# Optimization experiments

Hardware: AMD Instinct MI355X
Metric: run time of the kernel (lower is better)

## Reference

```python
import jax, jax.numpy as jnp
import numpy as np

D_MODEL = 1024
N_HEADS = 16
CAUSAL = True
NEG_INF = -1e10


def get_freqs(seq_len, n_dim):
    # standard RoPE frequencies: theta_i = 10000^(-2i/n_dim), angles[s, i] = s * theta_i
    inv_freq = 1.0 / (10000.0 ** (jnp.arange(0, n_dim, 2, dtype=jnp.float32) / n_dim))
    t = jnp.arange(seq_len, dtype=jnp.float32)
    return jnp.outer(t, inv_freq)  # [S, n_dim//2]


def rope(x, freqs):
    # x: [B, S, H, n_dim]; interleaved pair rotation
    B, S, H, Dh = x.shape
    xr = x.reshape(B, S, H, Dh // 2, 2)
    x1, x2 = xr[..., 0], xr[..., 1]
    cos = jnp.cos(freqs)[None, :, None, :]  # [1,S,1,Dh/2]
    sin = jnp.sin(freqs)[None, :, None, :]
    o1 = x1 * cos - x2 * sin
    o2 = x1 * sin + x2 * cos
    return jnp.stack([o1, o2], axis=-1).reshape(B, S, H, Dh)


def setup_inputs() -> dict:
    key = jax.random.key(0)
    ks = jax.random.split(key, 5)
    B, S, D = 2, 2048, D_MODEL
    return {
        "x": jax.random.normal(ks[0], (B, S, D), dtype=jnp.float32),
        "qw": jax.random.normal(ks[1], (D, D), dtype=jnp.float32),
        "kw": jax.random.normal(ks[2], (D, D), dtype=jnp.float32),
        "vw": jax.random.normal(ks[3], (D, D), dtype=jnp.float32),
        "ow": jax.random.normal(ks[4], (D, D), dtype=jnp.float32),
    }


def reference(x, qw, kw, vw, ow):
    B, S, D = x.shape
    H = N_HEADS
    Dh = D // H
    Q = (x @ qw).reshape(B, S, H, Dh)
    K = (x @ kw).reshape(B, S, H, Dh)
    V = (x @ vw).reshape(B, S, H, Dh)
    freqs = get_freqs(S, Dh)
    Q = rope(Q, freqs)
    K = rope(K, freqs)
    # [B,H,S,S] scores, scaled by sqrt(d_model) as in the original (not sqrt(head_dim))
    scores = jnp.einsum("bqhd,bkhd->bhqk", Q, K) / jnp.sqrt(jnp.float32(D))
    scores = scores.astype(jnp.float32)
    if CAUSAL:
        causal = jnp.tril(jnp.ones((S, S), dtype=bool))
        scores = jnp.where(causal[None, None, :, :], scores, NEG_INF)
    weights = jax.nn.softmax(scores, axis=-1)
    attn = jnp.einsum("bhqk,bkhd->bqhd", weights, V).reshape(B, S, D)
    return attn @ ow
```

## Files before the change

kernel.cpp:

```cpp
#include <hip/hip_runtime.h>
#include <hip/hip_bf16.h>
#include <math.h>

#define SEQ    2048
#define BATCH  2
#define DM     1024
#define NH     16
#define DH     64
#define BS_ROWS 4096
#define KDIM   1024

typedef __attribute__((ext_vector_type(8))) short short8v;
typedef __attribute__((ext_vector_type(4))) float f32x4;
typedef unsigned short ushort_t;

__device__ __forceinline__ unsigned short f2bf(float f) {
  union { float f; unsigned u; } v; v.f = f;
  unsigned r = (v.u + 0x7FFF + ((v.u >> 16) & 1)) >> 16;
  return (unsigned short)r;
}
__device__ __forceinline__ float bf2f(unsigned short h) {
  union { unsigned u; float f; } v; v.u = ((unsigned)h) << 16;
  return v.f;
}

__device__ __forceinline__ void gl16(const void* g, void* l) {
  __builtin_amdgcn_global_load_lds(
      (const __attribute__((address_space(1))) unsigned int*)g,
      (__attribute__((address_space(3))) unsigned int*)l,
      16, 0, 0);
}

__global__ __launch_bounds__(256)
void split_f32(const float* __restrict__ src, ushort_t* __restrict__ h,
               ushort_t* __restrict__ l, int n8)
{
  const int i = blockIdx.x * 256 + threadIdx.x;
  if (i >= n8) return;
  const float4 v0 = ((const float4*)src)[2 * i];
  const float4 v1 = ((const float4*)src)[2 * i + 1];
  const float vals[8] = {v0.x, v0.y, v0.z, v0.w, v1.x, v1.y, v1.z, v1.w};
  short8v hv, lv;
  #pragma unroll
  for (int e = 0; e < 8; e++) {
    const unsigned short hb = f2bf(vals[e]);
    hv[e] = (short)hb;
    lv[e] = (short)f2bf(vals[e] - bf2f(hb));
  }
  ((short8v*)h)[i] = hv;
  ((short8v*)l)[i] = lv;
}

__global__ __launch_bounds__(256)
void wtrans(const float* __restrict__ w0, const float* __restrict__ w1,
            const float* __restrict__ w2, const float* __restrict__ w3,
            ushort_t* __restrict__ WT)
{
  __shared__ float tile[64][65];
  const int z = blockIdx.z;
  const float* __restrict__ W = (z == 0) ? w0 : (z == 1) ? w1 : (z == 2) ? w2 : w3;
  ushort_t* __restrict__ Oh = WT + (size_t)z * 2097152;
  ushort_t* __restrict__ Ol = Oh + 1048576;

  const int n0 = blockIdx.x * 64, k0 = blockIdx.y * 64;
  const int r  = threadIdx.x >> 2;
  const int c0 = (threadIdx.x & 3) * 16;

  #pragma unroll
  for (int i = 0; i < 4; i++) {
    const float4 v = *(const float4*)&W[(size_t)(k0 + r) * KDIM + n0 + c0 + 4 * i];
    tile[r][c0 + 4 * i + 0] = v.x; tile[r][c0 + 4 * i + 1] = v.y;
    tile[r][c0 + 4 * i + 2] = v.z; tile[r][c0 + 4 * i + 3] = v.w;
  }
  __syncthreads();

  #pragma unroll
  for (int c = 0; c < 2; c++) {
    short8v hv, lv;
    #pragma unroll
    for (int e = 0; e < 8; e++) {
      const float x = tile[c0 + c * 8 + e][r];
      const unsigned short hb = f2bf(x);
      hv[e] = (short)hb;
      lv[e] = (short)f2bf(x - bf2f(hb));
    }
    const size_t off = (size_t)(n0 + r) * KDIM + k0 + c0 + c * 8;
    *(short8v*)&Oh[off] = hv;
    if (z <= 2) *(short8v*)&Ol[off] = lv;
  }
}

#define MF(a_, b_, c_) __builtin_amdgcn_mfma_f32_16x16x32_bf16(a_, b_, c_, 0, 0, 0)

#define M16(p_, q_)                                                          \
  c00=MF(p_##0,q_##0,c00); c01=MF(p_##0,q_##1,c01); c02=MF(p_##0,q_##2,c02); c03=MF(p_##0,q_##3,c03); \
  c10=MF(p_##1,q_##0,c10); c11=MF(p_##1,q_##1,c11); c12=MF(p_##1,q_##2,c12); c13=MF(p_##1,q_##3,c13); \
  c20=MF(p_##2,q_##0,c20); c21=MF(p_##2,q_##1,c21); c22=MF(p_##2,q_##2,c22); c23=MF(p_##2,q_##3,c23); \
  c30=MF(p_##3,q_##0,c30); c31=MF(p_##3,q_##1,c31); c32=MF(p_##3,q_##2,c32); c33=MF(p_##3,q_##3,c33);

__global__ __launch_bounds__(256, 2)
void gemm_qkv(const ushort_t* __restrict__ Ahp, const ushort_t* __restrict__ Alp,
              const ushort_t* __restrict__ WT,
              ushort_t* __restrict__ Qh, ushort_t* __restrict__ Ql,
              ushort_t* __restrict__ Kh, ushort_t* __restrict__ Kl,
              ushort_t* __restrict__ Vt)
{
  const int mode = blockIdx.z;
  const bool qk = (mode <= 1);
  const ushort_t* __restrict__ Bhp = WT + (size_t)mode * 2097152;
  const ushort_t* __restrict__ Blp = Bhp + 1048576;

  __shared__ ushort_t A2[128][64];
  __shared__ ushort_t B2[128][64];

  const int t = threadIdx.x;
  const int lane = t & 63, w = t >> 6;
  const int l4 = lane & 15, lh = lane >> 4;
  const int wm = w >> 1, wn = w & 1;

  const int lin = blockIdx.x + (blockIdx.y << 3);
  const int sw  = ((lin & 7) << 5) + (lin >> 3);
  const int row0 = (sw >> 3) * 128, col0 = (sw & 7) * 128;

  const int srow = t >> 3;
  const int spc  = t & 7;
  const int slc  = spc ^ (srow & 7);
  const int koff = (slc & 3) * 8;
  const ushort_t* __restrict__ sA = (slc < 4) ? Ahp : Alp;
  const ushort_t* __restrict__ sB = (slc < 4) ? Bhp : (qk ? Blp : Bhp);

  const int pcA = lh ^ (l4 & 7);

  f32x4 c00 = {0,0,0,0}, c01 = {0,0,0,0}, c02 = {0,0,0,0}, c03 = {0,0,0,0};
  f32x4 c10 = {0,0,0,0}, c11 = {0,0,0,0}, c12 = {0,0,0,0}, c13 = {0,0,0,0};
  f32x4 c20 = {0,0,0,0}, c21 = {0,0,0,0}, c22 = {0,0,0,0}, c23 = {0,0,0,0};
  f32x4 c30 = {0,0,0,0}, c31 = {0,0,0,0}, c32 = {0,0,0,0}, c33 = {0,0,0,0};

  const int rA = wm * 64 + l4;
  const int rB = wn * 64 + l4;

  for (int k0 = 0; k0 < KDIM; k0 += 32) {
    #pragma unroll
    for (int i = 0; i < 4; i++) {
      gl16(sA + (size_t)(row0 + i * 32 + srow) * KDIM + k0 + koff,
           (char*)A2 + i * 4096 + w * 1024);
      gl16(sB + (size_t)(col0 + i * 32 + srow) * KDIM + k0 + koff,
           (char*)B2 + i * 4096 + w * 1024);
    }
    __syncthreads();

    const short8v ah0 = *(const short8v*)&A2[rA +  0][pcA * 8];
    const short8v ah1 = *(const short8v*)&A2[rA + 16][pcA * 8];
    const short8v ah2 = *(const short8v*)&A2[rA + 32][pcA * 8];
    const short8v ah3 = *(const short8v*)&A2[rA + 48][pcA * 8];
    const short8v al0 = *(const short8v*)&A2[rA +  0][(pcA ^ 4) * 8];
    const short8v al1 = *(const short8v*)&A2[rA + 16][(pcA ^ 4) * 8];
    const short8v al2 = *(const short8v*)&A2[rA + 32][(pcA ^ 4) * 8];
    const short8v al3 = *(const short8v*)&A2[rA + 48][(pcA ^ 4) * 8];
    const short8v bh0 = *(const short8v*)&B2[rB +  0][pcA * 8];
    const short8v bh1 = *(const short8v*)&B2[rB + 16][pcA * 8];
    const short8v bh2 = *(const short8v*)&B2[rB + 32][pcA * 8];
    const short8v bh3 = *(const short8v*)&B2[rB + 48][pcA * 8];

    M16(ah, bh)
    if (qk) {
      const short8v bl0 = *(const short8v*)&B2[rB +  0][(pcA ^ 4) * 8];
      const short8v bl1 = *(const short8v*)&B2[rB + 16][(pcA ^ 4) * 8];
      const short8v bl2 = *(const short8v*)&B2[rB + 32][(pcA ^ 4) * 8];
      const short8v bl3 = *(const short8v*)&B2[rB + 48][(pcA ^ 4) * 8];
      M16(ah, bl)
    }
    M16(al, bh)
    __syncthreads();
  }

  f32x4 acc[4][4];
  acc[0][0]=c00; acc[0][1]=c01; acc[0][2]=c02; acc[0][3]=c03;
  acc[1][0]=c10; acc[1][1]=c11; acc[1][2]=c12; acc[1][3]=c13;
  acc[2][0]=c20; acc[2][1]=c21; acc[2][2]=c22; acc[2][3]=c23;
  acc[3][0]=c30; acc[3][1]=c31; acc[3][2]=c32; acc[3][3]=c33;

  if (mode <= 1) {
    const float scale = (mode == 0) ? 0.03125f : 1.0f;
    ushort_t* __restrict__ Hp = (mode == 0) ? Qh : Kh;
    ushort_t* __restrict__ Lp = (mode == 0) ? Ql : Kl;
    #pragma unroll
    for (int mf = 0; mf < 4; mf++)
      #pragma unroll
      for (int nf = 0; nf < 4; nf++) {
        const int col = col0 + wn * 64 + nf * 16 + l4;
        const int p = (col & (DH - 1)) >> 1;
        const float fr = exp2f((float)p * -0.41524101186092030f);
        const float sgn = (col & 1) ? 1.0f : -1.0f;
        #pragma unroll
        for (int j = 0; j < 4; j++) {
          const int grow = row0 + wm * 64 + mf * 16 + lh * 4 + j;
          const float s = (float)(grow & (SEQ - 1));
          float sn, cs;
          sincosf(s * fr, &sn, &cs);
          const float val = acc[mf][nf][j];
          const float par = __shfl_xor(val, 1);
          const float out = val * cs + par * (sgn * sn);
          const float xsc = out * scale;
          const unsigned short hb = f2bf(xsc);
          Hp[(size_t)grow * DM + col] = hb;
          Lp[(size_t)grow * DM + col] = f2bf(xsc - bf2f(hb));
        }
      }
  } else {
    #pragma unroll
    for (int mf = 0; mf < 4; mf++)
      #pragma unroll
      for (int nf = 0; nf < 4; nf++) {
        const int col = col0 + wn * 64 + nf * 16 + l4;
        const int hh = col >> 6, dd = col & (DH - 1);
        #pragma unroll
        for (int j = 0; j < 4; j++) {
          const int grow = row0 + wm * 64 + mf * 16 + lh * 4 + j;
          const int b = grow >> 11, ss = grow & (SEQ - 1);
          Vt[((size_t)((b * NH + hh) * DH + dd)) * SEQ + ss] = f2bf(acc[mf][nf][j]);
        }
      }
  }
}

__global__ __launch_bounds__(256, 2)
void gemm_out(const ushort_t* __restrict__ Ahp, const ushort_t* __restrict__ WT,
              float* __restrict__ Cf)
{
  const ushort_t* __restrict__ Bhp = WT + (size_t)3 * 2097152;

  __shared__ ushort_t A3[128][32];
  __shared__ ushort_t B3[64][32];

  const int t = threadIdx.x;
  const int lane = t & 63, w = t >> 6;
  const int l4 = lane & 15, lh = lane >> 4;
  const int wm = w >> 1, wn = w & 1;

  const int lin = blockIdx.x + (blockIdx.y << 4);
  const int sw  = ((lin & 7) << 6) + (lin >> 3);
  const int row0 = (sw >> 4) * 128, col0 = (sw & 15) * 64;

  const int srow = t >> 2;
  const int spc  = t & 3;
  const int slc  = spc ^ (srow & 3);
  const int koff = slc * 8;

  const int pc4 = lh ^ (l4 & 3);

  f32x4 c00={0,0,0,0}, c01={0,0,0,0};
  f32x4 c10={0,0,0,0}, c11={0,0,0,0};
  f32x4 c20={0,0,0,0}, c21={0,0,0,0};
  f32x4 c30={0,0,0,0}, c31={0,0,0,0};

  const int rA = wm * 64 + l4;
  const int rB = wn * 32 + l4;

  for (int k0 = 0; k0 < KDIM; k0 += 32) {
    #pragma unroll
    for (int i = 0; i < 2; i++)
      gl16(Ahp + (size_t)(row0 + i * 64 + srow) * KDIM + k0 + koff,
           (char*)A3 + i * 4096 + w * 1024);
    gl16(Bhp + (size_t)(col0 + srow) * KDIM + k0 + koff,
         (char*)B3 + w * 1024);
    __syncthreads();

    const short8v ah0 = *(const short8v*)&A3[rA +  0][pc4 * 8];
    const short8v ah1 = *(const short8v*)&A3[rA + 16][pc4 * 8];
    const short8v ah2 = *(const short8v*)&A3[rA + 32][pc4 * 8];
    const short8v ah3 = *(const short8v*)&A3[rA + 48][pc4 * 8];
    const short8v bh0 = *(const short8v*)&B3[rB +  0][pc4 * 8];
    const short8v bh1 = *(const short8v*)&B3[rB + 16][pc4 * 8];

    c00 = MF(ah0, bh0, c00); c01 = MF(ah0, bh1, c01);
    c10 = MF(ah1, bh0, c10); c11 = MF(ah1, bh1, c11);
    c20 = MF(ah2, bh0, c20); c21 = MF(ah2, bh1, c21);
    c30 = MF(ah3, bh0, c30); c31 = MF(ah3, bh1, c31);
    __syncthreads();
  }

  f32x4 acc[4][2];
  acc[0][0]=c00; acc[0][1]=c01; acc[1][0]=c10; acc[1][1]=c11;
  acc[2][0]=c20; acc[2][1]=c21; acc[3][0]=c30; acc[3][1]=c31;

  #pragma unroll
  for (int mf = 0; mf < 4; mf++)
    #pragma unroll
    for (int nf = 0; nf < 2; nf++) {
      const int col = col0 + wn * 32 + nf * 16 + l4;
      #pragma unroll
      for (int j = 0; j < 4; j++) {
        const int grow = row0 + wm * 64 + mf * 16 + lh * 4 + j;
        Cf[(size_t)grow * DM + col] = acc[mf][nf][j];
      }
    }
}

__global__ __launch_bounds__(256, 4)
void attn_mfma(const ushort_t* __restrict__ Qh, const ushort_t* __restrict__ Ql,
               const ushort_t* __restrict__ Kh, const ushort_t* __restrict__ Kl,
               const ushort_t* __restrict__ Vt, ushort_t* __restrict__ AAh)
{
  __shared__ __align__(16) ushort_t Khl[2][2][64][32];
  __shared__ __align__(16) ushort_t Vtl[64][72];
  __shared__ __align__(16) ushort_t Pl[4][16][72];

  const int t = threadIdx.x;
  const int lane = t & 63, wv = t >> 6;
  const int l4 = lane & 15, lh = lane >> 4;
  const int qblk = blockIdx.x, bh = blockIdx.y;
  const int bI = bh >> 4, h = bh & 15;
  const int q0w = qblk * 64 + wv * 16;
  const int qrow = q0w + l4;

  const int kr = t >> 2, kc = t & 3;
  const int ckw = (kc ^ ((kr >> 1) & 3)) * 8;
  const int csr = (lh ^ ((l4 >> 1) & 3)) * 8;

  short8v aqh0, aqh1, aql0, aql1;
  {
    const size_t qoff = (size_t)((bI * SEQ) + qrow) * DM + h * DH;
    aqh0 = *(const short8v*)&Qh[qoff + lh * 8];
    aqh1 = *(const short8v*)&Qh[qoff + 32 + lh * 8];
    aql0 = *(const short8v*)&Ql[qoff + lh * 8];
    aql1 = *(const short8v*)&Ql[qoff + 32 + lh * 8];
  }

  f32x4 o0 = {0,0,0,0}, o1 = {0,0,0,0}, o2 = {0,0,0,0}, o3 = {0,0,0,0};
  float mrun = -1e30f, lsum = 0.f;

  const ushort_t* __restrict__ Vg = Vt + (size_t)bh * DH * SEQ;
  const size_t kgbase = (size_t)(bI * SEQ + kr) * DM + h * DH + kc * 8;
  const int nt = qblk + 1;

  short8v rkh0, rkh1, rkl0, rkl1, rv0, rv1;

#define LOADR(kt_) {                                                         \
    const size_t ko = kgbase + (size_t)(kt_) * 64 * DM;                      \
    rkh0 = *(const short8v*)&Kh[ko];                                         \
    rkh1 = *(const short8v*)&Kh[ko + 32];                                    \
    rkl0 = *(const short8v*)&Kl[ko];                                         \
    rkl1 = *(const short8v*)&Kl[ko + 32];                                    \
    const size_t vo = (size_t)kr * SEQ + (kt_) * 64 + kc * 8;                \
    rv0 = *(const short8v*)&Vg[vo];                                          \
    rv1 = *(const short8v*)&Vg[vo + 32]; }

#define WRITES() {                                                           \
    *(short8v*)&Khl[0][0][kr][ckw] = rkh0;                                   \
    *(short8v*)&Khl[0][1][kr][ckw] = rkh1;                                   \
    *(short8v*)&Khl[1][0][kr][ckw] = rkl0;                                   \
    *(short8v*)&Khl[1][1][kr][ckw] = rkl1;                                   \
    *(short8v*)&Vtl[kr][kc * 8]      = rv0;                                  \
    *(short8v*)&Vtl[kr][kc * 8 + 32] = rv1; }

#define QKSTEP(sN, n) {                                                      \
    const short8v kh0 = *(const short8v*)&Khl[0][0][(n)*16 + l4][csr];       \
    const short8v kh1 = *(const short8v*)&Khl[0][1][(n)*16 + l4][csr];       \
    const short8v kl0 = *(const short8v*)&Khl[1][0][(n)*16 + l4][csr];       \
    const short8v kl1 = *(const short8v*)&Khl[1][1][(n)*16 + l4][csr];       \
    sN = MF(kh0, aqh0, sN);                                                  \
    sN = MF(kh0, aql0, sN);                                                  \
    sN = MF(kl0, aqh0, sN);                                                  \
    sN = MF(kh1, aqh1, sN);                                                  \
    sN = MF(kh1, aql1, sN);                                                  \
    sN = MF(kl1, aqh1, sN); }

#define MASKN(sN, n) {                                                       \
    const int kb0 = kb + (n)*16 + lh*4;                                      \
    if (kb0 + 0 > qrow) sN[0] = -1e30f;                                      \
    if (kb0 + 1 > qrow) sN[1] = -1e30f;                                      \
    if (kb0 + 2 > qrow) sN[2] = -1e30f;                                      \
    if (kb0 + 3 > qrow) sN[3] = -1e30f; }

#define EXPN(sN) {                                                           \
    sN[0] = __expf(sN[0] - nm); sN[1] = __expf(sN[1] - nm);                  \
    sN[2] = __expf(sN[2] - nm); sN[3] = __expf(sN[3] - nm); }

#define PWRITE(sN, n) {                                                      \
    unsigned pa, pb;                                                         \
    asm("v_cvt_pk_bf16_f32 %0, %1, %2" : "=v"(pa) : "v"(sN[0]), "v"(sN[1]));\
    asm("v_cvt_pk_bf16_f32 %0, %1, %2" : "=v"(pb) : "v"(sN[2]), "v"(sN[3]));\
    *(unsigned*)&Pl[wv][l4][(n)*16 + lh*4]     = pa;                         \
    *(unsigned*)&Pl[wv][l4][(n)*16 + lh*4 + 2] = pb; }

#define PVSTEP(kb2) {                                                        \
    const short8v ap  = *(const short8v*)&Pl[wv][l4][(kb2)*32 + lh*8];       \
    const short8v bv0 = *(const short8v*)&Vtl[ 0 + l4][(kb2)*32 + lh*8];     \
    const short8v bv1 = *(const short8v*)&Vtl[16 + l4][(kb2)*32 + lh*8];     \
    const short8v bv2 = *(const short8v*)&Vtl[32 + l4][(kb2)*32 + lh*8];     \
    const short8v bv3 = *(const short8v*)&Vtl[48 + l4][(kb2)*32 + lh*8];     \
    o0 = MF(bv0, ap, o0);                                                    \
    o1 = MF(bv1, ap, o1);                                                    \
    o2 = MF(bv2, ap, o2);                                                    \
    o3 = MF(bv3, ap, o3); }

  LOADR(0); WRITES();
  __syncthreads();

  for (int kt = 0; kt < nt; kt++) {
    const bool pf = (kt + 1 < nt);
    if (pf) LOADR(kt + 1);

    f32x4 s0 = {0,0,0,0}, s1 = {0,0,0,0}, s2 = {0,0,0,0}, s3 = {0,0,0,0};
    QKSTEP(s0, 0) QKSTEP(s1, 1) QKSTEP(s2, 2) QKSTEP(s3, 3)

    const int kb = kt * 64;
    MASKN(s0, 0) MASKN(s1, 1) MASKN(s2, 2) MASKN(s3, 3)

    float vmax = fmaxf(fmaxf(fmaxf(s0[0], s0[1]), fmaxf(s0[2], s0[3])),
                       fmaxf(fmaxf(s1[0], s1[1]), fmaxf(s1[2], s1[3])));
    vmax = fmaxf(vmax, fmaxf(fmaxf(s2[0], s2[1]), fmaxf(s2[2], s2[3])));
    vmax = fmaxf(vmax, fmaxf(fmaxf(s3[0], s3[1]), fmaxf(s3[2], s3[3])));
    vmax = fmaxf(vmax, __shfl_xor(vmax, 16));
    vmax = fmaxf(vmax, __shfl_xor(vmax, 32));

    const float nm = fmaxf(mrun, vmax);
    const float corr = __expf(mrun - nm);
    mrun = nm;

    EXPN(s0) EXPN(s1) EXPN(s2) EXPN(s3)

    float rs = (s0[0] + s0[1]) + (s0[2] + s0[3]) + (s1[0] + s1[1]) + (s1[2] + s1[3])
             + (s2[0] + s2[1]) + (s2[2] + s2[3]) + (s3[0] + s3[1]) + (s3[2] + s3[3]);
    rs += __shfl_xor(rs, 16);
    rs += __shfl_xor(rs, 32);
    lsum = lsum * corr + rs;

    o0 *= corr; o1 *= corr; o2 *= corr; o3 *= corr;

    PWRITE(s0, 0) PWRITE(s1, 1) PWRITE(s2, 2) PWRITE(s3, 3)

    PVSTEP(0) PVSTEP(1)

    if (pf) {
      __syncthreads();
      WRITES();
      __syncthreads();
    }
  }

  const float inv = 1.0f / lsum;
  const size_t rowoff = ((size_t)(bI * SEQ + qrow)) * DM + h * DH;
  #pragma unroll
  for (int df = 0; df < 4; df++) {
    const f32x4 ov = (df == 0) ? o0 : (df == 1) ? o1 : (df == 2) ? o2 : o3;
    #pragma unroll
    for (int jp = 0; jp < 2; jp++) {
      const float x0 = ov[2 * jp] * inv;
      const float x1 = ov[2 * jp + 1] * inv;
      const unsigned short h0 = f2bf(x0), h1 = f2bf(x1);
      const size_t col = rowoff + df * 16 + lh * 4 + 2 * jp;
      *(unsigned*)&AAh[col] = (unsigned)h0 | ((unsigned)h1 << 16);
    }
  }
#undef LOADR
#undef WRITES
#undef QKSTEP
#undef MASKN
#undef EXPN
#undef PWRITE
#undef PVSTEP
}

extern "C" void kernel_launch(void* const* d_in, const int* in_sizes, int n_in,
                              void* d_out, int out_size, void* d_ws, size_t ws_size,
                              hipStream_t stream) {
  const float* x  = (const float*)d_in[0];
  const float* qw = (const float*)d_in[1];
  const float* kw = (const float*)d_in[2];
  const float* vw = (const float*)d_in[3];
  const float* ow = (const float*)d_in[4];

  char* ws = (char*)d_ws;
  ushort_t* Xh  = (ushort_t*)ws;
  ushort_t* Xl  = Xh + 4194304;
  ushort_t* AAh = Xh;
  ushort_t* Kh  = (ushort_t*)(ws + (16u << 20));
  ushort_t* Kl  = Kh + 4194304;
  ushort_t* Vt  = (ushort_t*)(ws + (32u << 20));
  ushort_t* WT  = (ushort_t*)(ws + (40u << 20));
  ushort_t* Qh  = (ushort_t*)d_out;
  ushort_t* Ql  = Qh + 4194304;
  float*    out = (float*)d_out;

  split_f32<<<dim3(2048), dim3(256), 0, stream>>>(x, Xh, Xl, 524288);
  wtrans<<<dim3(16, 16, 4), dim3(256), 0, stream>>>(qw, kw, vw, ow, WT);
  gemm_qkv<<<dim3(8, 32, 3), dim3(256), 0, stream>>>(
      Xh, Xl, WT, Qh, Ql, Kh, Kl, Vt);
  attn_mfma<<<dim3(SEQ / 64, BATCH * NH), dim3(256), 0, stream>>>(
      Qh, Ql, Kh, Kl, Vt, AAh);
  gemm_out<<<dim3(16, 32), dim3(256), 0, stream>>>(AAh, WT, out);
}
```

Baseline: 208.3 us.

## Prefetch next K tile into registers while computing current tile in GEMM

Replaces the direct global-to-LDS loads (gl16) in the projection GEMM main loop with register staging. The next K-slice is loaded into registers before the MFMAs on the current slice run, then written to LDS after a barrier. The goal is to hide global memory latency behind compute. The cost is extra VGPRs, which may lower occupancy, an extra barrier per iteration, and an LDS write pass that the direct-to-LDS path avoided.

```diff
diff --git a/kernel.cpp b/kernel.cpp
--- a/kernel.cpp
+++ b/kernel.cpp
@@ -139,15 +139,34 @@
   const int rA = wm * 64 + l4;
   const int rB = wn * 64 + l4;
 
-  for (int k0 = 0; k0 < KDIM; k0 += 32) {
-    #pragma unroll
-    for (int i = 0; i < 4; i++) {
-      gl16(sA + (size_t)(row0 + i * 32 + srow) * KDIM + k0 + koff,
-           (char*)A2 + i * 4096 + w * 1024);
-      gl16(sB + (size_t)(col0 + i * 32 + srow) * KDIM + k0 + koff,
-           (char*)B2 + i * 4096 + w * 1024);
-    }
-    __syncthreads();
+  short8v ra0, ra1, ra2, ra3, rb0, rb1, rb2, rb3;
+
+#define LOADR(k0_) {                                                         \
+    ra0 = *(const short8v*)&sA[(size_t)(row0 +  0 + srow) * KDIM + (k0_) + koff]; \
+    ra1 = *(const short8v*)&sA[(size_t)(row0 + 32 + srow) * KDIM + (k0_) + koff]; \
+    ra2 = *(const short8v*)&sA[(size_t)(row0 + 64 + srow) * KDIM + (k0_) + koff]; \
+    ra3 = *(const short8v*)&sA[(size_t)(row0 + 96 + srow) * KDIM + (k0_) + koff]; \
+    rb0 = *(const short8v*)&sB[(size_t)(col0 +  0 + srow) * KDIM + (k0_) + koff]; \
+    rb1 = *(const short8v*)&sB[(size_t)(col0 + 32 + srow) * KDIM + (k0_) + koff]; \
+    rb2 = *(const short8v*)&sB[(size_t)(col0 + 64 + srow) * KDIM + (k0_) + koff]; \
+    rb3 = *(const short8v*)&sB[(size_t)(col0 + 96 + srow) * KDIM + (k0_) + koff]; }
+
+#define WRITES() {                                                           \
+    *(short8v*)&A2[ 0 + srow][spc * 8] = ra0;                                \
+    *(short8v*)&A2[32 + srow][spc * 8] = ra1;                                \
+    *(short8v*)&A2[64 + srow][spc * 8] = ra2;                                \
+    *(short8v*)&A2[96 + srow][spc * 8] = ra3;                                \
+    *(short8v*)&B2[ 0 + srow][spc * 8] = rb0;                                \
+    *(short8v*)&B2[32 + srow][spc * 8] = rb1;                                \
+    *(short8v*)&B2[64 + srow][spc * 8] = rb2;                                \
+    *(short8v*)&B2[96 + srow][spc * 8] = rb3; }
+
+  LOADR(0); WRITES();
+  __syncthreads();
+
+  for (int kt = 0; kt < 32; kt++) {
+    const bool pf = (kt + 1 < 32);
+    if (pf) LOADR((kt + 1) * 32);
 
     const short8v ah0 = *(const short8v*)&A2[rA +  0][pcA * 8];
     const short8v ah1 = *(const short8v*)&A2[rA + 16][pcA * 8];
@@ -171,8 +190,15 @@
       M16(ah, bl)
     }
     M16(al, bh)
+
     __syncthreads();
-  }
+    if (pf) {
+      WRITES();
+      __syncthreads();
+    }
+  }
+#undef LOADR
+#undef WRITES
 
   f32x4 acc[4][4];
   acc[0][0]=c00; acc[0][1]=c01; acc[0][2]=c02; acc[0][3]=c03;
```

After: 210.4 us. Within noise of the previous version (+1.0%).
